# Performance work log

Hardware: AMD Instinct MI355X
Metric: run time of the kernel (lower is better)

Reference implementation:

```python
import jax, jax.numpy as jnp
import numpy as np

LEVELS = (4, 3, 2, 1)
EMBED = 4096


def _spp(x):
    # adaptive max pool to n x n per level (H,W divisible by every level), concat
    N, C, H, W = x.shape
    feats = []
    for n in LEVELS:
        p = x.reshape(N, C, n, H // n, n, W // n).max(axis=(3, 5))
        feats.append(p.reshape(N, C * n * n))
    return jnp.concatenate(feats, axis=1)  # (N, 90)


def _lstm_cell(x, h, c, wih, whh, bih, bhh):
    # torch gate order: i, f, g, o
    g = x @ wih.T + bih + h @ whh.T + bhh
    i, f, gg, o = jnp.split(g, 4, axis=-1)
    c2 = jax.nn.sigmoid(f) * c + jax.nn.sigmoid(i) * jnp.tanh(gg)
    h2 = jax.nn.sigmoid(o) * jnp.tanh(c2)
    return h2, c2


def _lin_init(key, out_d, in_d):
    k = 1.0 / np.sqrt(in_d)
    kw, kb = jax.random.split(key)
    w = jax.random.uniform(kw, (out_d, in_d), jnp.float32, -k, k)
    b = jax.random.uniform(kb, (out_d,), jnp.float32, -k, k)
    return w, b


def setup_inputs() -> dict:
    key = jax.random.key(0)
    ks = jax.random.split(key, 9)
    frames = jax.random.normal(ks[0], (8, 256, 3, 96, 96), jnp.float32)
    spp_fc_w, spp_fc_b = _lin_init(ks[1], EMBED, 90)
    fc7_w, fc7_b = _lin_init(ks[2], 64, EMBED)
    forecast_w, forecast_b = _lin_init(ks[3], 90, 32)
    fc8_w, fc8_b = _lin_init(ks[4], 1, 32)
    lstm1_wih, lstm1_bih = _lin_init(ks[5], 256, 64)
    lstm1_whh, lstm1_bhh = _lin_init(ks[6], 256, 64)
    lstm2_wih, lstm2_bih = _lin_init(ks[7], 128, 64)
    lstm2_whh, lstm2_bhh = _lin_init(ks[8], 128, 32)
    return dict(frames=frames, spp_fc_w=spp_fc_w, spp_fc_b=spp_fc_b,
                fc7_w=fc7_w, fc7_b=fc7_b,
                lstm1_wih=lstm1_wih, lstm1_whh=lstm1_whh, lstm1_bih=lstm1_bih, lstm1_bhh=lstm1_bhh,
                lstm2_wih=lstm2_wih, lstm2_whh=lstm2_whh, lstm2_bih=lstm2_bih, lstm2_bhh=lstm2_bhh,
                forecast_w=forecast_w, forecast_b=forecast_b, fc8_w=fc8_w, fc8_b=fc8_b)


def reference(frames, spp_fc_w, spp_fc_b, fc7_w, fc7_b,
              lstm1_wih, lstm1_whh, lstm1_bih, lstm1_bhh,
              lstm2_wih, lstm2_whh, lstm2_bih, lstm2_bhh,
              forecast_w, forecast_b, fc8_w, fc8_b):
    B, S, C, H, W = frames.shape
    pooled = _spp(frames.reshape(B * S, C, H, W))               # (B*S, 90)
    emb = jax.nn.relu(pooled @ spp_fc_w.T + spp_fc_b)           # (B*S, 4096)
    emb = jax.nn.relu(emb @ fc7_w.T + fc7_b).reshape(B, S, -1)  # (B, S, 64)

    def step(carry, e):
        h1, c1, h2, c2 = carry
        h1n, c1n = _lstm_cell(e, h1, c1, lstm1_wih, lstm1_whh, lstm1_bih, lstm1_bhh)
        h2n, c2n = _lstm_cell(h1n, h2, c2, lstm2_wih, lstm2_whh, lstm2_bih, lstm2_bhh)
        fpool = h2n @ forecast_w.T + forecast_b                  # (B, 90)
        fe = jax.nn.relu(fpool @ spp_fc_w.T + spp_fc_b)
        fe = jax.nn.relu(fe @ fc7_w.T + fc7_b)
        fh1, _ = _lstm_cell(fe, h1n, c1n, lstm1_wih, lstm1_whh, lstm1_bih, lstm1_bhh)
        fh2, _ = _lstm_cell(fh1, h2n, c2n, lstm2_wih, lstm2_whh, lstm2_bih, lstm2_bhh)
        return (h1n, c1n, h2n, c2n), (h2n, fh2, fpool)

    z = lambda d: jnp.zeros((B, d), frames.dtype)
    init = (z(64), z(64), z(32), z(32))
    _, (prog, fprog, fpooled) = jax.lax.scan(step, init, jnp.swapaxes(emb, 0, 1))
    prog = jnp.swapaxes(prog, 0, 1)        # (B, S, 32)
    fprog = jnp.swapaxes(fprog, 0, 1)      # (B, S, 32)
    fpooled = jnp.swapaxes(fpooled, 0, 1)  # (B, S, 90)
    progress = jax.nn.sigmoid(prog @ fc8_w.T + fc8_b)[..., 0]    # (B, S)
    fprogress = jax.nn.sigmoid(fprog @ fc8_w.T + fc8_b)[..., 0]  # (B, S)
    return (progress, fprogress, pooled.reshape(B, S, -1), fpooled)
```

## Files before the change

kernel.cpp:

```cpp
#include <hip/hip_runtime.h>
#include <math.h>

static const size_t OFF_POOLED = 0;
static const size_t OFF_EMB1   = 184320;
static const size_t OFF_ACC1   = OFF_EMB1 + 8388608;
static const size_t OFF_ACC2   = OFF_ACC1 + 131072;
static const size_t OFF_X1     = OFF_ACC2 + 131072;
static const size_t OFF_FPOOL  = OFF_X1 + 524288;
static const size_t OFF_H1     = OFF_FPOOL + 184320;
static const size_t OFF_C1     = OFF_H1 + 131072;
static const size_t OFF_H2     = OFF_C1 + 131072;
static const size_t OFF_C2     = OFF_H2 + 65536;

typedef _Float16 h2f_t __attribute__((ext_vector_type(2)));

__device__ __forceinline__ float fsig(float x) {
    return __builtin_amdgcn_rcpf(1.0f + __expf(-x));
}
__device__ __forceinline__ float ftanh(float x) {
    return 1.0f - 2.0f * __builtin_amdgcn_rcpf(__expf(2.0f * x) + 1.0f);
}

__device__ __forceinline__ float fdot2(h2f_t a, h2f_t b, float c) {
#if __has_builtin(__builtin_amdgcn_fdot2)
    return __builtin_amdgcn_fdot2(a, b, c, false);
#else
    return c + (float)a.x * (float)b.x + (float)a.y * (float)b.y;
#endif
}
__device__ __forceinline__ h2f_t h2pack(float x, float y) {
    h2f_t r; r.x = (_Float16)x; r.y = (_Float16)y; return r;
}
__device__ __forceinline__ h2f_t h2bits(int v) {
    return __builtin_bit_cast(h2f_t, v);
}
__device__ __forceinline__ void lds_fence() {
    asm volatile("s_waitcnt lgkmcnt(0)" ::: "memory");
}

__global__ __launch_bounds__(256) void spp_kernel(const float* __restrict__ frames,
                                                  float* __restrict__ out_pooled,
                                                  float* __restrict__ ws_pooled) {
    __shared__ __align__(16) float img[9216];
    __shared__ float p4[16], p3[9];
    int blk = blockIdx.x;
    int n = blk / 3, c = blk % 3;
    const float* src = frames + (size_t)blk * 9216;
    int tid = threadIdx.x;
    const float4* s4 = (const float4*)src;
    float4* i4 = (float4*)img;
#pragma unroll
    for (int j = 0; j < 9; ++j) i4[tid + 256 * j] = s4[tid + 256 * j];
    __syncthreads();
    {
        int r = tid >> 4, i = tid & 15;
        int ri = r >> 2, rj = r & 3;
        const float* base = &img[(24 * ri) * 96 + 24 * rj];
        float m = -3.402823466e38f;
#pragma unroll 6
        for (int k = 0; k < 36; ++k) {
            int e = i + 16 * k;
            int row = e / 24;
            int col = e - row * 24;
            m = fmaxf(m, base[row * 96 + col]);
        }
#pragma unroll
        for (int sh = 8; sh >= 1; sh >>= 1) m = fmaxf(m, __shfl_xor(m, sh));
        if (i == 0) p4[r] = m;
    }
    if (tid < 144) {
        int r = tid >> 4, i = tid & 15;
        int ri = r / 3, rj = r % 3;
        const float* base = &img[(32 * ri) * 96 + 32 * rj];
        float m = -3.402823466e38f;
#pragma unroll 8
        for (int k = 0; k < 64; ++k) {
            int e = i + 16 * k;
            int row = e >> 5, col = e & 31;
            m = fmaxf(m, base[row * 96 + col]);
        }
#pragma unroll
        for (int sh = 8; sh >= 1; sh >>= 1) m = fmaxf(m, __shfl_xor(m, sh));
        if (i == 0) p3[r] = m;
    }
    __syncthreads();
    if (tid < 30) {
        float v; int off;
        if (tid < 16) { v = p4[tid]; off = c * 16 + tid; }
        else if (tid < 25) { int q = tid - 16; v = p3[q]; off = 48 + c * 9 + q; }
        else if (tid < 29) {
            int q = tid - 25; int i2 = q >> 1, j2 = q & 1;
            v = fmaxf(fmaxf(p4[(2 * i2) * 4 + 2 * j2], p4[(2 * i2) * 4 + 2 * j2 + 1]),
                      fmaxf(p4[(2 * i2 + 1) * 4 + 2 * j2], p4[(2 * i2 + 1) * 4 + 2 * j2 + 1]));
            off = 75 + c * 4 + q;
        } else {
            float m = p4[0];
#pragma unroll
            for (int q = 1; q < 16; ++q) m = fmaxf(m, p4[q]);
            v = m; off = 87 + c;
        }
        out_pooled[(size_t)n * 90 + off] = v;
        ws_pooled[(size_t)n * 90 + off] = v;
    }
}

__global__ __launch_bounds__(256) void gemm90_kernel(const float* __restrict__ X,
                                                     const float* __restrict__ W,
                                                     const float* __restrict__ bias,
                                                     float* __restrict__ Y) {
    __shared__ __align__(16) float Xs[32][132];
    __shared__ __align__(16) float Ws[32][132];
    int tid = threadIdx.x;
    int R0 = blockIdx.x * 128, C0 = blockIdx.y * 128;
    int r0t = (tid >> 4) * 8, c0t = (tid & 15) * 8;
    float acc[8][8];
#pragma unroll
    for (int i = 0; i < 8; ++i)
#pragma unroll
        for (int j = 0; j < 8; ++j) acc[i][j] = 0.f;

    for (int k0 = 0; k0 < 96; k0 += 32) {
#pragma unroll
        for (int j = 0; j < 4; ++j) {
            int idx = tid + 256 * j;
            int row = idx & 127, q = idx >> 7;
            int kg = k0 + 4 * q;
            const float2* p = (const float2*)&X[(size_t)(R0 + row) * 90 + kg];
            float2 a = p[0], b = p[1];
            Xs[4 * q + 0][row] = a.x; Xs[4 * q + 1][row] = a.y;
            Xs[4 * q + 2][row] = b.x; Xs[4 * q + 3][row] = b.y;
        }
#pragma unroll
        for (int j = 0; j < 4; ++j) {
            int idx = tid + 256 * j;
            int col = idx & 127, q = idx >> 7;
            int kg = k0 + 4 * q;
            float v0, v1, v2, v3;
            if (kg + 3 < 90) {
                const float2* p = (const float2*)&W[(size_t)(C0 + col) * 90 + kg];
                float2 a = p[0], b = p[1];
                v0 = a.x; v1 = a.y; v2 = b.x; v3 = b.y;
            } else {
                const float* p = &W[(size_t)(C0 + col) * 90];
                v0 = (kg + 0 < 90) ? p[kg + 0] : 0.f;
                v1 = (kg + 1 < 90) ? p[kg + 1] : 0.f;
                v2 = (kg + 2 < 90) ? p[kg + 2] : 0.f;
                v3 = (kg + 3 < 90) ? p[kg + 3] : 0.f;
            }
            Ws[4 * q + 0][col] = v0; Ws[4 * q + 1][col] = v1;
            Ws[4 * q + 2][col] = v2; Ws[4 * q + 3][col] = v3;
        }
        __syncthreads();
#pragma unroll 8
        for (int kk = 0; kk < 32; ++kk) {
            float4 xa = *(const float4*)&Xs[kk][r0t];
            float4 xb = *(const float4*)&Xs[kk][r0t + 4];
            float4 wa = *(const float4*)&Ws[kk][c0t];
            float4 wb = *(const float4*)&Ws[kk][c0t + 4];
            float xr[8] = {xa.x, xa.y, xa.z, xa.w, xb.x, xb.y, xb.z, xb.w};
            float wc[8] = {wa.x, wa.y, wa.z, wa.w, wb.x, wb.y, wb.z, wb.w};
#pragma unroll
            for (int i = 0; i < 8; ++i)
#pragma unroll
                for (int j = 0; j < 8; ++j) acc[i][j] += xr[i] * wc[j];
        }
        __syncthreads();
    }
    float4 ba = *(const float4*)&bias[C0 + c0t];
    float4 bb = *(const float4*)&bias[C0 + c0t + 4];
    float bs[8] = {ba.x, ba.y, ba.z, ba.w, bb.x, bb.y, bb.z, bb.w};
#pragma unroll
    for (int i = 0; i < 8; ++i) {
        float4 o0, o1;
        o0.x = fmaxf(acc[i][0] + bs[0], 0.f); o0.y = fmaxf(acc[i][1] + bs[1], 0.f);
        o0.z = fmaxf(acc[i][2] + bs[2], 0.f); o0.w = fmaxf(acc[i][3] + bs[3], 0.f);
        o1.x = fmaxf(acc[i][4] + bs[4], 0.f); o1.y = fmaxf(acc[i][5] + bs[5], 0.f);
        o1.z = fmaxf(acc[i][6] + bs[6], 0.f); o1.w = fmaxf(acc[i][7] + bs[7], 0.f);
        *(float4*)&Y[(size_t)(R0 + r0t + i) * 4096 + C0 + c0t] = o0;
        *(float4*)&Y[(size_t)(R0 + r0t + i) * 4096 + C0 + c0t + 4] = o1;
    }
}

__global__ __launch_bounds__(256) void gemmk_kernel(const float* __restrict__ X,
                                                    const float* __restrict__ W,
                                                    float* __restrict__ acc_out) {
    __shared__ __align__(16) float Xs[32][132];
    __shared__ __align__(16) float Ws[32][68];
    int tid = threadIdx.x;
    int R0 = blockIdx.x * 128;
    int K0 = blockIdx.y * 256;
    int r0t = (tid >> 4) * 8, c0t = (tid & 15) * 4;
    float acc[8][4];
#pragma unroll
    for (int i = 0; i < 8; ++i)
#pragma unroll
        for (int j = 0; j < 4; ++j) acc[i][j] = 0.f;

    for (int k0 = K0; k0 < K0 + 256; k0 += 32) {
#pragma unroll
        for (int j = 0; j < 4; ++j) {
            int idx = tid + 256 * j;
            int row = idx & 127, q = idx >> 7;
            float4 a = *(const float4*)&X[(size_t)(R0 + row) * 4096 + k0 + 4 * q];
            Xs[4 * q + 0][row] = a.x; Xs[4 * q + 1][row] = a.y;
            Xs[4 * q + 2][row] = a.z; Xs[4 * q + 3][row] = a.w;
        }
#pragma unroll
        for (int j = 0; j < 2; ++j) {
            int idx = tid + 256 * j;
            int col = idx & 63, q = idx >> 6;
            float4 a = *(const float4*)&W[(size_t)col * 4096 + k0 + 4 * q];
            Ws[4 * q + 0][col] = a.x; Ws[4 * q + 1][col] = a.y;
            Ws[4 * q + 2][col] = a.z; Ws[4 * q + 3][col] = a.w;
        }
        __syncthreads();
#pragma unroll 8
        for (int kk = 0; kk < 32; ++kk) {
            float4 xa = *(const float4*)&Xs[kk][r0t];
            float4 xb = *(const float4*)&Xs[kk][r0t + 4];
            float4 wa = *(const float4*)&Ws[kk][c0t];
            float xr[8] = {xa.x, xa.y, xa.z, xa.w, xb.x, xb.y, xb.z, xb.w};
            float wc[4] = {wa.x, wa.y, wa.z, wa.w};
#pragma unroll
            for (int i = 0; i < 8; ++i)
#pragma unroll
                for (int j = 0; j < 4; ++j) acc[i][j] += xr[i] * wc[j];
        }
        __syncthreads();
    }
#pragma unroll
    for (int i = 0; i < 8; ++i)
#pragma unroll
        for (int j = 0; j < 4; ++j)
            atomicAdd(&acc_out[(size_t)(R0 + r0t + i) * 64 + c0t + j], acc[i][j]);
}

__global__ __launch_bounds__(256) void x1_kernel(const float* __restrict__ acc1,
                                                 const float* __restrict__ fc7_b,
                                                 const float* __restrict__ wih1,
                                                 const float* __restrict__ bih1,
                                                 const float* __restrict__ bhh1,
                                                 float* __restrict__ X1) {
    __shared__ __align__(16) float xr[8][64];
    int tid = threadIdx.x;
    int R0 = blockIdx.x * 8;
#pragma unroll
    for (int j = 0; j < 2; ++j) {
        int idx = tid + 256 * j;
        int r = idx >> 6, k = idx & 63;
        xr[r][k] = fmaxf(acc1[(size_t)(R0 + r) * 64 + k] + fc7_b[k], 0.f);
    }
    __syncthreads();
    int u = tid;
    float w[64];
#pragma unroll
    for (int q = 0; q < 16; ++q) {
        float4 a = *(const float4*)&wih1[(size_t)u * 64 + 4 * q];
        w[4 * q] = a.x; w[4 * q + 1] = a.y; w[4 * q + 2] = a.z; w[4 * q + 3] = a.w;
    }
    float bias = bih1[u] + bhh1[u];
    for (int r = 0; r < 8; ++r) {
        float g = bias;
#pragma unroll
        for (int k = 0; k < 64; ++k) g += w[k] * xr[r][k];
        X1[(size_t)(R0 + r) * 256 + u] = g;
    }
}

__global__ __launch_bounds__(64, 1) void seq_kernel(const float* __restrict__ X1,
                                                    const float* __restrict__ whh1,
                                                    const float* __restrict__ wih2,
                                                    const float* __restrict__ whh2,
                                                    const float* __restrict__ bih2,
                                                    const float* __restrict__ bhh2,
                                                    float* __restrict__ h1_all, float* __restrict__ c1_all,
                                                    float* __restrict__ h2_all, float* __restrict__ c2_all) {
    __shared__ __align__(16) _Float16 h1h[64];
    __shared__ __align__(16) _Float16 h2h[32];
    const int l = threadIdx.x;
    const size_t n0 = (size_t)blockIdx.x * 256;

    h2f_t w1[4][32];
#pragma unroll
    for (int g = 0; g < 4; ++g) {
        const float* wr = whh1 + (size_t)(g * 64 + l) * 64;
#pragma unroll
        for (int q = 0; q < 32; ++q) w1[g][q] = h2pack(wr[2 * q], wr[2 * q + 1]);
    }
    h2f_t w2a[2][32], w2b[2][16];
#pragma unroll
    for (int g = 0; g < 2; ++g) {
        const float* wa = wih2 + (size_t)(g * 64 + l) * 64;
#pragma unroll
        for (int q = 0; q < 32; ++q) w2a[g][q] = h2pack(wa[2 * q], wa[2 * q + 1]);
        const float* wb = whh2 + (size_t)(g * 64 + l) * 32;
#pragma unroll
        for (int q = 0; q < 16; ++q) w2b[g][q] = h2pack(wb[2 * q], wb[2 * q + 1]);
    }
    const float b2a = bih2[l] + bhh2[l];
    const float b2b = bih2[64 + l] + bhh2[64 + l];

    const float* xp = X1 + n0 * 256;
    float c1, c2 = 0.f, pa, pb;
    {
        float a0 = xp[l], a1 = xp[64 + l], a2 = xp[128 + l], a3 = xp[192 + l];
        (void)a1;
        c1 = fsig(a0) * ftanh(a2);
        float h1n = fsig(a3) * ftanh(c1);
        h1h[l] = (_Float16)h1n;
        h1_all[n0 * 64 + l] = h1n;
        c1_all[n0 * 64 + l] = c1;
        pa = b2a; pb = b2b;
    }
    lds_fence();
    float xb0[4], xb1[4];
    {
        const float* x1r = xp + 256;
        xb0[0] = x1r[l]; xb0[1] = x1r[64 + l]; xb0[2] = x1r[128 + l]; xb0[3] = x1r[192 + l];
        const float* x2r = xp + 512;
        xb1[0] = x2r[l]; xb1[1] = x2r[64 + l]; xb1[2] = x2r[128 + l]; xb1[3] = x2r[192 + l];
    }

#pragma unroll 2
    for (int t = 0; t < 256; ++t) {
        int4 hv[8];
        const int4* h1v = (const int4*)h1h;
#pragma unroll
        for (int q = 0; q < 8; ++q) hv[q] = h1v[q];
        float* xc = (t & 1) ? xb1 : xb0;
        float a0 = xc[0], a1 = xc[1], a2 = xc[2], a3 = xc[3];
        {
            int tr = (t + 3 < 256) ? (t + 3) : 255;
            const float* xq = xp + (size_t)tr * 256;
            xc[0] = xq[l]; xc[1] = xq[64 + l]; xc[2] = xq[128 + l]; xc[3] = xq[192 + l];
        }
#pragma unroll
        for (int q = 0; q < 8; ++q) {
            int4 v = hv[q];
            h2f_t hh0 = h2bits(v.x), hh1 = h2bits(v.y), hh2 = h2bits(v.z), hh3 = h2bits(v.w);
            a0 = fdot2(w1[0][4 * q], hh0, a0); a1 = fdot2(w1[1][4 * q], hh0, a1);
            a2 = fdot2(w1[2][4 * q], hh0, a2); a3 = fdot2(w1[3][4 * q], hh0, a3);
            pa = fdot2(w2a[0][4 * q], hh0, pa); pb = fdot2(w2a[1][4 * q], hh0, pb);
            a0 = fdot2(w1[0][4 * q + 1], hh1, a0); a1 = fdot2(w1[1][4 * q + 1], hh1, a1);
            a2 = fdot2(w1[2][4 * q + 1], hh1, a2); a3 = fdot2(w1[3][4 * q + 1], hh1, a3);
            pa = fdot2(w2a[0][4 * q + 1], hh1, pa); pb = fdot2(w2a[1][4 * q + 1], hh1, pb);
            a0 = fdot2(w1[0][4 * q + 2], hh2, a0); a1 = fdot2(w1[1][4 * q + 2], hh2, a1);
            a2 = fdot2(w1[2][4 * q + 2], hh2, a2); a3 = fdot2(w1[3][4 * q + 2], hh2, a3);
            pa = fdot2(w2a[0][4 * q + 2], hh2, pa); pb = fdot2(w2a[1][4 * q + 2], hh2, pb);
            a0 = fdot2(w1[0][4 * q + 3], hh3, a0); a1 = fdot2(w1[1][4 * q + 3], hh3, a1);
            a2 = fdot2(w1[2][4 * q + 3], hh3, a2); a3 = fdot2(w1[3][4 * q + 3], hh3, a3);
            pa = fdot2(w2a[0][4 * q + 3], hh3, pa); pb = fdot2(w2a[1][4 * q + 3], hh3, pb);
        }
        float gf_ = __shfl(pa, (l & 31) + 32);
        float go_ = __shfl(pb, (l & 31) + 32);
        if (l < 32) {
            c2 = fsig(gf_) * c2 + fsig(pa) * ftanh(pb);
            float h2n = fsig(go_) * ftanh(c2);
            h2h[l] = (_Float16)h2n;
            h2_all[(n0 + t) * 32 + l] = h2n;
            c2_all[(n0 + t) * 32 + l] = c2;
        }
        lds_fence();
        c1 = fsig(a1) * c1 + fsig(a0) * ftanh(a2);
        float h1n = fsig(a3) * ftanh(c1);
        h1h[l] = (_Float16)h1n;
        if (t < 255) {
            h1_all[(n0 + t + 1) * 64 + l] = h1n;
            c1_all[(n0 + t + 1) * 64 + l] = c1;
        }
        pa = b2a; pb = b2b;
        const int4* h2v = (const int4*)h2h;
#pragma unroll
        for (int q = 0; q < 4; ++q) {
            int4 v = h2v[q];
            h2f_t hh0 = h2bits(v.x), hh1 = h2bits(v.y), hh2 = h2bits(v.z), hh3 = h2bits(v.w);
            pa = fdot2(w2b[0][4 * q], hh0, pa); pb = fdot2(w2b[1][4 * q], hh0, pb);
            pa = fdot2(w2b[0][4 * q + 1], hh1, pa); pb = fdot2(w2b[1][4 * q + 1], hh1, pb);
            pa = fdot2(w2b[0][4 * q + 2], hh2, pa); pb = fdot2(w2b[1][4 * q + 2], hh2, pb);
            pa = fdot2(w2b[0][4 * q + 3], hh3, pa); pb = fdot2(w2b[1][4 * q + 3], hh3, pb);
        }
        lds_fence();
    }
}

__global__ __launch_bounds__(256) void fpool_kernel(const float* __restrict__ h2_all,
                                                    const float* __restrict__ fw,
                                                    const float* __restrict__ fb,
                                                    const float* __restrict__ fc8_w,
                                                    const float* __restrict__ fc8_b,
                                                    float* __restrict__ fpool_ws,
                                                    float* __restrict__ out_fpooled,
                                                    float* __restrict__ out_progress) {
    __shared__ __align__(16) float h2t[16][32];
    __shared__ float fwl[2880];
    int tid = threadIdx.x;
    int R0 = blockIdx.x * 16;
#pragma unroll
    for (int j = 0; j < 2; ++j) {
        int idx = tid + 256 * j;
        int r = idx >> 5, k = idx & 31;
        h2t[r][k] = h2_all[(size_t)(R0 + r) * 32 + k];
    }
    for (int idx = tid; idx < 2880; idx += 256) fwl[idx] = fw[idx];
    __syncthreads();
    for (int j = 0; j < 6; ++j) {
        int idx = tid + 256 * j;
        if (idx < 1440) {
            int r = idx / 90, cc = idx % 90;
            float g = fb[cc];
#pragma unroll
            for (int k = 0; k < 32; ++k) g += h2t[r][k] * fwl[cc * 32 + k];
            fpool_ws[(size_t)(R0 + r) * 90 + cc] = g;
            out_fpooled[(size_t)(R0 + r) * 90 + cc] = g;
        }
    }
    if (tid < 16) {
        float g = fc8_b[0];
#pragma unroll
        for (int k = 0; k < 32; ++k) g += h2t[tid][k] * fc8_w[k];
        out_progress[R0 + tid] = fsig(g);
    }
}

__global__ __launch_bounds__(256) void fh_kernel(const float* __restrict__ acc2,
                                                 const float* __restrict__ fc7_b,
                                                 const float* __restrict__ h1_all,
                                                 const float* __restrict__ c1_all,
                                                 const float* __restrict__ h2_all,
                                                 const float* __restrict__ c2_all,
                                                 const float* __restrict__ wih1,
                                                 const float* __restrict__ whh1,
                                                 const float* __restrict__ bih1,
                                                 const float* __restrict__ bhh1,
                                                 const float* __restrict__ wih2,
                                                 const float* __restrict__ whh2,
                                                 const float* __restrict__ bih2,
                                                 const float* __restrict__ bhh2,
                                                 const float* __restrict__ fc8_w,
                                                 const float* __restrict__ fc8_b,
                                                 float* __restrict__ out_fprog) {
    __shared__ __align__(16) float xcat[8][128];
    __shared__ float g1f[8][256];
    __shared__ __align__(16) float x2c[8][96];
    __shared__ float g2f[8][128];
    __shared__ __align__(16) float fh2s[8][32];
    int tid = threadIdx.x;
    int R0 = blockIdx.x * 8;
#pragma unroll
    for (int j = 0; j < 4; ++j) {
        int idx = tid + 256 * j;
        int r = idx >> 7, k = idx & 127;
        float v;
        if (k < 64) v = fmaxf(acc2[(size_t)(R0 + r) * 64 + k] + fc7_b[k], 0.f);
        else v = h1_all[(size_t)(R0 + r) * 64 + (k - 64)];
        xcat[r][k] = v;
    }
    {
        int r = tid >> 5, k = tid & 31;
        x2c[r][64 + k] = h2_all[(size_t)(R0 + r) * 32 + k];
    }
    __syncthreads();
    {
        int u = tid;
        float wa[64], wb[64];
#pragma unroll
        for (int q = 0; q < 16; ++q) {
            float4 a = *(const float4*)&wih1[(size_t)u * 64 + 4 * q];
            wa[4 * q] = a.x; wa[4 * q + 1] = a.y; wa[4 * q + 2] = a.z; wa[4 * q + 3] = a.w;
            float4 b = *(const float4*)&whh1[(size_t)u * 64 + 4 * q];
            wb[4 * q] = b.x; wb[4 * q + 1] = b.y; wb[4 * q + 2] = b.z; wb[4 * q + 3] = b.w;
        }
        float bias = bih1[u] + bhh1[u];
        for (int r = 0; r < 8; ++r) {
            float g = bias;
#pragma unroll
            for (int k = 0; k < 64; ++k) g += wa[k] * xcat[r][k];
#pragma unroll
            for (int k = 0; k < 64; ++k) g += wb[k] * xcat[r][64 + k];
            g1f[r][u] = g;
        }
    }
    __syncthreads();
#pragma unroll
    for (int j = 0; j < 2; ++j) {
        int idx = tid + 256 * j;
        int r = idx >> 6, h = idx & 63;
        float gi = g1f[r][h], gf = g1f[r][64 + h], gg = g1f[r][128 + h], go = g1f[r][192 + h];
        float c1v = c1_all[(size_t)(R0 + r) * 64 + h];
        float c = fsig(gf) * c1v + fsig(gi) * ftanh(gg);
        x2c[r][h] = fsig(go) * ftanh(c);
    }
    __syncthreads();
    {
        int u = tid & 127;
        int rb = (tid >> 7) * 4;
        float wa[64], wb2[32];
#pragma unroll
        for (int q = 0; q < 16; ++q) {
            float4 a = *(const float4*)&wih2[(size_t)u * 64 + 4 * q];
            wa[4 * q] = a.x; wa[4 * q + 1] = a.y; wa[4 * q + 2] = a.z; wa[4 * q + 3] = a.w;
        }
#pragma unroll
        for (int q = 0; q < 8; ++q) {
            float4 b = *(const float4*)&whh2[(size_t)u * 32 + 4 * q];
            wb2[4 * q] = b.x; wb2[4 * q + 1] = b.y; wb2[4 * q + 2] = b.z; wb2[4 * q + 3] = b.w;
        }
        float bias = bih2[u] + bhh2[u];
        for (int r = rb; r < rb + 4; ++r) {
            float g = bias;
#pragma unroll
            for (int k = 0; k < 64; ++k) g += wa[k] * x2c[r][k];
#pragma unroll
            for (int k = 0; k < 32; ++k) g += wb2[k] * x2c[r][64 + k];
            g2f[r][u] = g;
        }
    }
    __syncthreads();
    {
        int r = tid >> 5, v = tid & 31;
        float gi = g2f[r][v], gf = g2f[r][32 + v], gg = g2f[r][64 + v], go = g2f[r][96 + v];
        float c2v = c2_all[(size_t)(R0 + r) * 32 + v];
        float c = fsig(gf) * c2v + fsig(gi) * ftanh(gg);
        fh2s[r][v] = fsig(go) * ftanh(c);
    }
    __syncthreads();
    if (tid < 8) {
        float g = fc8_b[0];
#pragma unroll
        for (int k = 0; k < 32; ++k) g += fh2s[tid][k] * fc8_w[k];
        out_fprog[R0 + tid] = fsig(g);
    }
}

extern "C" void kernel_launch(void* const* d_in, const int* in_sizes, int n_in,
                              void* d_out, int out_size, void* d_ws, size_t ws_size,
                              hipStream_t stream) {
    (void)in_sizes; (void)n_in; (void)out_size; (void)ws_size;
    const float* frames   = (const float*)d_in[0];
    const float* spp_fc_w = (const float*)d_in[1];
    const float* spp_fc_b = (const float*)d_in[2];
    const float* fc7_w    = (const float*)d_in[3];
    const float* fc7_b    = (const float*)d_in[4];
    const float* l1_wih   = (const float*)d_in[5];
    const float* l1_whh   = (const float*)d_in[6];
    const float* l1_bih   = (const float*)d_in[7];
    const float* l1_bhh   = (const float*)d_in[8];
    const float* l2_wih   = (const float*)d_in[9];
    const float* l2_whh   = (const float*)d_in[10];
    const float* l2_bih   = (const float*)d_in[11];
    const float* l2_bhh   = (const float*)d_in[12];
    const float* fo_w     = (const float*)d_in[13];
    const float* fo_b     = (const float*)d_in[14];
    const float* fc8_w    = (const float*)d_in[15];
    const float* fc8_b    = (const float*)d_in[16];
    float* out = (float*)d_out;
    float* ws  = (float*)d_ws;

    float* pooled = ws + OFF_POOLED;
    float* emb1   = ws + OFF_EMB1;
    float* acc1   = ws + OFF_ACC1;
    float* acc2   = ws + OFF_ACC2;
    float* X1     = ws + OFF_X1;
    float* fpool  = ws + OFF_FPOOL;
    float* h1a    = ws + OFF_H1;
    float* c1a    = ws + OFF_C1;
    float* h2a    = ws + OFF_H2;
    float* c2a    = ws + OFF_C2;

    float* out_prog    = out;
    float* out_fprog   = out + 2048;
    float* out_pooled  = out + 4096;
    float* out_fpooled = out + 188416;

    hipMemsetAsync(acc1, 0, (size_t)262144 * sizeof(float), stream);
    spp_kernel<<<6144, 256, 0, stream>>>(frames, out_pooled, pooled);
    gemm90_kernel<<<dim3(16, 32), 256, 0, stream>>>(pooled, spp_fc_w, spp_fc_b, emb1);
    gemmk_kernel<<<dim3(16, 16), 256, 0, stream>>>(emb1, fc7_w, acc1);
    x1_kernel<<<256, 256, 0, stream>>>(acc1, fc7_b, l1_wih, l1_bih, l1_bhh, X1);
    seq_kernel<<<8, 64, 0, stream>>>(X1, l1_whh, l2_wih, l2_whh, l2_bih, l2_bhh, h1a, c1a, h2a, c2a);
    fpool_kernel<<<128, 256, 0, stream>>>(h2a, fo_w, fo_b, fc8_w, fc8_b, fpool, out_fpooled, out_prog);
    gemm90_kernel<<<dim3(16, 32), 256, 0, stream>>>(fpool, spp_fc_w, spp_fc_b, emb1);
    gemmk_kernel<<<dim3(16, 16), 256, 0, stream>>>(emb1, fc7_w, acc2);
    fh_kernel<<<256, 256, 0, stream>>>(acc2, fc7_b, h1a, c1a, h2a, c2a,
                                       l1_wih, l1_whh, l1_bih, l1_bhh,
                                       l2_wih, l2_whh, l2_bih, l2_bhh,
                                       fc8_w, fc8_b, out_fprog);
}
```

Baseline: 769.1 us.

## Split sequential LSTM kernel into two wavefronts pipelining layer 1 and layer 2

The sequential LSTM kernel now launches 128 threads. One wavefront runs the layer-1 recurrence and writes h1 into a double-buffered LDS slot. The second wavefront computes layer 2 for the previous step, and the two hand off through per-step barriers. Dot products are split across several independent accumulators to shorten dependency chains, and v_permlane32_swap replaces the shuffles used to gather gates. This takes layer-2 work off the layer-1 critical path, at the cost of a workgroup barrier every timestep and reliance on the correctness of the partial lgkmcnt wait.

```diff
diff --git a/kernel.cpp b/kernel.cpp
--- a/kernel.cpp
+++ b/kernel.cpp
@@ -36,6 +36,9 @@
 }
 __device__ __forceinline__ void lds_fence() {
     asm volatile("s_waitcnt lgkmcnt(0)" ::: "memory");
+}
+__device__ __forceinline__ void permswap(float& x, float& y) {
+    asm volatile("v_permlane32_swap_b32 %0, %1" : "+v"(x), "+v"(y));
 }
 
 __global__ __launch_bounds__(256) void spp_kernel(const float* __restrict__ frames,
@@ -267,119 +270,171 @@
     }
 }
 
-__global__ __launch_bounds__(64, 1) void seq_kernel(const float* __restrict__ X1,
-                                                    const float* __restrict__ whh1,
-                                                    const float* __restrict__ wih2,
-                                                    const float* __restrict__ whh2,
-                                                    const float* __restrict__ bih2,
-                                                    const float* __restrict__ bhh2,
-                                                    float* __restrict__ h1_all, float* __restrict__ c1_all,
-                                                    float* __restrict__ h2_all, float* __restrict__ c2_all) {
-    __shared__ __align__(16) _Float16 h1h[64];
+__global__ __launch_bounds__(128, 1) void seq_kernel(const float* __restrict__ X1,
+                                                     const float* __restrict__ whh1,
+                                                     const float* __restrict__ wih2,
+                                                     const float* __restrict__ whh2,
+                                                     const float* __restrict__ bih2,
+                                                     const float* __restrict__ bhh2,
+                                                     float* __restrict__ h1_all, float* __restrict__ c1_all,
+                                                     float* __restrict__ h2_all, float* __restrict__ c2_all) {
+    __shared__ __align__(16) _Float16 h1h[2][64];
     __shared__ __align__(16) _Float16 h2h[32];
-    const int l = threadIdx.x;
+    const int tid = threadIdx.x;
+    const int l = tid & 63;
     const size_t n0 = (size_t)blockIdx.x * 256;
-
-    h2f_t w1[4][32];
-#pragma unroll
-    for (int g = 0; g < 4; ++g) {
-        const float* wr = whh1 + (size_t)(g * 64 + l) * 64;
-#pragma unroll
-        for (int q = 0; q < 32; ++q) w1[g][q] = h2pack(wr[2 * q], wr[2 * q + 1]);
-    }
-    h2f_t w2a[2][32], w2b[2][16];
-#pragma unroll
-    for (int g = 0; g < 2; ++g) {
-        const float* wa = wih2 + (size_t)(g * 64 + l) * 64;
-#pragma unroll
-        for (int q = 0; q < 32; ++q) w2a[g][q] = h2pack(wa[2 * q], wa[2 * q + 1]);
-        const float* wb = whh2 + (size_t)(g * 64 + l) * 32;
-#pragma unroll
-        for (int q = 0; q < 16; ++q) w2b[g][q] = h2pack(wb[2 * q], wb[2 * q + 1]);
-    }
-    const float b2a = bih2[l] + bhh2[l];
-    const float b2b = bih2[64 + l] + bhh2[64 + l];
-
     const float* xp = X1 + n0 * 256;
-    float c1, c2 = 0.f, pa, pb;
-    {
-        float a0 = xp[l], a1 = xp[64 + l], a2 = xp[128 + l], a3 = xp[192 + l];
-        (void)a1;
-        c1 = fsig(a0) * ftanh(a2);
-        float h1n = fsig(a3) * ftanh(c1);
-        h1h[l] = (_Float16)h1n;
-        h1_all[n0 * 64 + l] = h1n;
-        c1_all[n0 * 64 + l] = c1;
-        pa = b2a; pb = b2b;
-    }
-    lds_fence();
-    float xb0[4], xb1[4];
-    {
-        const float* x1r = xp + 256;
-        xb0[0] = x1r[l]; xb0[1] = x1r[64 + l]; xb0[2] = x1r[128 + l]; xb0[3] = x1r[192 + l];
-        const float* x2r = xp + 512;
-        xb1[0] = x2r[l]; xb1[1] = x2r[64 + l]; xb1[2] = x2r[128 + l]; xb1[3] = x2r[192 + l];
-    }
+
+    if (tid < 64) {
+        h2f_t w1[4][32];
+#pragma unroll
+        for (int g = 0; g < 4; ++g) {
+            const float* wr = whh1 + (size_t)(g * 64 + l) * 64;
+#pragma unroll
+            for (int q = 0; q < 32; ++q) w1[g][q] = h2pack(wr[2 * q], wr[2 * q + 1]);
+        }
+        float c1;
+        {
+            float a0 = xp[l], a1 = xp[64 + l], a2 = xp[128 + l], a3 = xp[192 + l];
+            (void)a1;
+            c1 = fsig(a0) * ftanh(a2);
+            float h1n = fsig(a3) * ftanh(c1);
+            h1h[0][l] = (_Float16)h1n;
+            h1_all[n0 * 64 + l] = h1n;
+            c1_all[n0 * 64 + l] = c1;
+        }
+        float xb0[4], xb1[4];
+        {
+            const float* x1r = xp + 256;
+            xb0[0] = x1r[l]; xb0[1] = x1r[64 + l]; xb0[2] = x1r[128 + l]; xb0[3] = x1r[192 + l];
+            const float* x2r = xp + 512;
+            xb1[0] = x2r[l]; xb1[1] = x2r[64 + l]; xb1[2] = x2r[128 + l]; xb1[3] = x2r[192 + l];
+        }
+        lds_fence();
+        int4 hv[8];
+        {
+            const int4* hb = (const int4*)&h1h[0][0];
+#pragma unroll
+            for (int q = 0; q < 8; ++q) hv[q] = hb[q];
+        }
+        __builtin_amdgcn_s_barrier();
 
 #pragma unroll 2
-    for (int t = 0; t < 256; ++t) {
-        int4 hv[8];
-        const int4* h1v = (const int4*)h1h;
-#pragma unroll
-        for (int q = 0; q < 8; ++q) hv[q] = h1v[q];
-        float* xc = (t & 1) ? xb1 : xb0;
-        float a0 = xc[0], a1 = xc[1], a2 = xc[2], a3 = xc[3];
+        for (int t = 0; t < 256; ++t) {
+            float* xc = (t & 1) ? xb1 : xb0;
+            float a0 = xc[0], a1 = xc[1], a2 = xc[2], a3 = xc[3];
+            {
+                int tr = (t + 3 < 256) ? (t + 3) : 255;
+                const float* xq = xp + (size_t)tr * 256;
+                xc[0] = xq[l]; xc[1] = xq[64 + l]; xc[2] = xq[128 + l]; xc[3] = xq[192 + l];
+            }
+            float b0 = 0.f, b1 = 0.f, b2 = 0.f, b3 = 0.f;
+#pragma unroll
+            for (int q = 0; q < 8; ++q) {
+                int4 v = hv[q];
+                h2f_t hh0 = h2bits(v.x), hh1 = h2bits(v.y), hh2 = h2bits(v.z), hh3 = h2bits(v.w);
+                a0 = fdot2(w1[0][4 * q], hh0, a0);     a1 = fdot2(w1[1][4 * q], hh0, a1);
+                a2 = fdot2(w1[2][4 * q], hh0, a2);     a3 = fdot2(w1[3][4 * q], hh0, a3);
+                b0 = fdot2(w1[0][4 * q + 1], hh1, b0); b1 = fdot2(w1[1][4 * q + 1], hh1, b1);
+                b2 = fdot2(w1[2][4 * q + 1], hh1, b2); b3 = fdot2(w1[3][4 * q + 1], hh1, b3);
+                a0 = fdot2(w1[0][4 * q + 2], hh2, a0); a1 = fdot2(w1[1][4 * q + 2], hh2, a1);
+                a2 = fdot2(w1[2][4 * q + 2], hh2, a2); a3 = fdot2(w1[3][4 * q + 2], hh2, a3);
+                b0 = fdot2(w1[0][4 * q + 3], hh3, b0); b1 = fdot2(w1[1][4 * q + 3], hh3, b1);
+                b2 = fdot2(w1[2][4 * q + 3], hh3, b2); b3 = fdot2(w1[3][4 * q + 3], hh3, b3);
+            }
+            a0 += b0; a1 += b1; a2 += b2; a3 += b3;
+            c1 = fsig(a1) * c1 + fsig(a0) * ftanh(a2);
+            float h1n = fsig(a3) * ftanh(c1);
+            h1h[(t + 1) & 1][l] = (_Float16)h1n;
+            if (t < 255) {
+                h1_all[(n0 + t + 1) * 64 + l] = h1n;
+                c1_all[(n0 + t + 1) * 64 + l] = c1;
+            }
+            {
+                const int4* hb = (const int4*)&h1h[(t + 1) & 1][0];
+#pragma unroll
+                for (int q = 0; q < 8; ++q) hv[q] = hb[q];
+            }
+            asm volatile("s_waitcnt lgkmcnt(8)" ::: "memory");
+            __builtin_amdgcn_s_barrier();
+        }
+    } else {
+        h2f_t w2a[2][32], w2b[2][16];
+#pragma unroll
+        for (int g = 0; g < 2; ++g) {
+            const float* wa = wih2 + (size_t)(g * 64 + l) * 64;
+#pragma unroll
+            for (int q = 0; q < 32; ++q) w2a[g][q] = h2pack(wa[2 * q], wa[2 * q + 1]);
+            const float* wb = whh2 + (size_t)(g * 64 + l) * 32;
+#pragma unroll
+            for (int q = 0; q < 16; ++q) w2b[g][q] = h2pack(wb[2 * q], wb[2 * q + 1]);
+        }
+        const float b2a = bih2[l] + bhh2[l];
+        const float b2b = bih2[64 + l] + bhh2[64 + l];
+        const bool hi = (l >= 32);
+        if (l < 32) h2h[l] = (_Float16)0.f;
+        lds_fence();
+        int4 gv[4];
         {
-            int tr = (t + 3 < 256) ? (t + 3) : 255;
-            const float* xq = xp + (size_t)tr * 256;
-            xc[0] = xq[l]; xc[1] = xq[64 + l]; xc[2] = xq[128 + l]; xc[3] = xq[192 + l];
-        }
-#pragma unroll
-        for (int q = 0; q < 8; ++q) {
-            int4 v = hv[q];
-            h2f_t hh0 = h2bits(v.x), hh1 = h2bits(v.y), hh2 = h2bits(v.z), hh3 = h2bits(v.w);
-            a0 = fdot2(w1[0][4 * q], hh0, a0); a1 = fdot2(w1[1][4 * q], hh0, a1);
-            a2 = fdot2(w1[2][4 * q], hh0, a2); a3 = fdot2(w1[3][4 * q], hh0, a3);
-            pa = fdot2(w2a[0][4 * q], hh0, pa); pb = fdot2(w2a[1][4 * q], hh0, pb);
-            a0 = fdot2(w1[0][4 * q + 1], hh1, a0); a1 = fdot2(w1[1][4 * q + 1], hh1, a1);
-            a2 = fdot2(w1[2][4 * q + 1], hh1, a2); a3 = fdot2(w1[3][4 * q + 1], hh1, a3);
-            pa = fdot2(w2a[0][4 * q + 1], hh1, pa); pb = fdot2(w2a[1][4 * q + 1], hh1, pb);
-            a0 = fdot2(w1[0][4 * q + 2], hh2, a0); a1 = fdot2(w1[1][4 * q + 2], hh2, a1);
-            a2 = fdot2(w1[2][4 * q + 2], hh2, a2); a3 = fdot2(w1[3][4 * q + 2], hh2, a3);
-            pa = fdot2(w2a[0][4 * q + 2], hh2, pa); pb = fdot2(w2a[1][4 * q + 2], hh2, pb);
-            a0 = fdot2(w1[0][4 * q + 3], hh3, a0); a1 = fdot2(w1[1][4 * q + 3], hh3, a1);
-            a2 = fdot2(w1[2][4 * q + 3], hh3, a2); a3 = fdot2(w1[3][4 * q + 3], hh3, a3);
-            pa = fdot2(w2a[0][4 * q + 3], hh3, pa); pb = fdot2(w2a[1][4 * q + 3], hh3, pb);
-        }
-        float gf_ = __shfl(pa, (l & 31) + 32);
-        float go_ = __shfl(pb, (l & 31) + 32);
-        if (l < 32) {
-            c2 = fsig(gf_) * c2 + fsig(pa) * ftanh(pb);
-            float h2n = fsig(go_) * ftanh(c2);
-            h2h[l] = (_Float16)h2n;
-            h2_all[(n0 + t) * 32 + l] = h2n;
-            c2_all[(n0 + t) * 32 + l] = c2;
-        }
-        lds_fence();
-        c1 = fsig(a1) * c1 + fsig(a0) * ftanh(a2);
-        float h1n = fsig(a3) * ftanh(c1);
-        h1h[l] = (_Float16)h1n;
-        if (t < 255) {
-            h1_all[(n0 + t + 1) * 64 + l] = h1n;
-            c1_all[(n0 + t + 1) * 64 + l] = c1;
-        }
-        pa = b2a; pb = b2b;
-        const int4* h2v = (const int4*)h2h;
-#pragma unroll
-        for (int q = 0; q < 4; ++q) {
-            int4 v = h2v[q];
-            h2f_t hh0 = h2bits(v.x), hh1 = h2bits(v.y), hh2 = h2bits(v.z), hh3 = h2bits(v.w);
-            pa = fdot2(w2b[0][4 * q], hh0, pa); pb = fdot2(w2b[1][4 * q], hh0, pb);
-            pa = fdot2(w2b[0][4 * q + 1], hh1, pa); pb = fdot2(w2b[1][4 * q + 1], hh1, pb);
-            pa = fdot2(w2b[0][4 * q + 2], hh2, pa); pb = fdot2(w2b[1][4 * q + 2], hh2, pb);
-            pa = fdot2(w2b[0][4 * q + 3], hh3, pa); pb = fdot2(w2b[1][4 * q + 3], hh3, pb);
-        }
-        lds_fence();
+            const int4* gb = (const int4*)&h2h[0];
+#pragma unroll
+            for (int q = 0; q < 4; ++q) gv[q] = gb[q];
+        }
+        float c2 = 0.f;
+        __builtin_amdgcn_s_barrier();
+
+        for (int t = 0; t < 256; ++t) {
+            int4 hv[8];
+            {
+                const int4* hb = (const int4*)&h1h[t & 1][0];
+#pragma unroll
+                for (int q = 0; q < 8; ++q) hv[q] = hb[q];
+            }
+            float pa = b2a, pb = b2b, pc = 0.f, pd = 0.f;
+            float pe = 0.f, pf = 0.f, pg = 0.f, ph = 0.f;
+#pragma unroll
+            for (int q = 0; q < 4; ++q) {
+                int4 u = gv[q];
+                h2f_t gg0 = h2bits(u.x), gg1 = h2bits(u.y), gg2 = h2bits(u.z), gg3 = h2bits(u.w);
+                pe = fdot2(w2b[0][4 * q], gg0, pe);     pf = fdot2(w2b[1][4 * q], gg0, pf);
+                pg = fdot2(w2b[0][4 * q + 1], gg1, pg); ph = fdot2(w2b[1][4 * q + 1], gg1, ph);
+                pe = fdot2(w2b[0][4 * q + 2], gg2, pe); pf = fdot2(w2b[1][4 * q + 2], gg2, pf);
+                pg = fdot2(w2b[0][4 * q + 3], gg3, pg); ph = fdot2(w2b[1][4 * q + 3], gg3, ph);
+            }
+#pragma unroll
+            for (int q = 0; q < 8; ++q) {
+                int4 v = hv[q];
+                h2f_t hh0 = h2bits(v.x), hh1 = h2bits(v.y), hh2 = h2bits(v.z), hh3 = h2bits(v.w);
+                pa = fdot2(w2a[0][4 * q], hh0, pa);     pb = fdot2(w2a[1][4 * q], hh0, pb);
+                pa = fdot2(w2a[0][4 * q + 1], hh1, pa); pb = fdot2(w2a[1][4 * q + 1], hh1, pb);
+                pc = fdot2(w2a[0][4 * q + 2], hh2, pc); pd = fdot2(w2a[1][4 * q + 2], hh2, pd);
+                pc = fdot2(w2a[0][4 * q + 3], hh3, pc); pd = fdot2(w2a[1][4 * q + 3], hh3, pd);
+            }
+            pa = (pa + pc) + (pe + pg);
+            pb = (pb + pd) + (pf + ph);
+            float s1a = pa, s1b = pb;
+            permswap(s1a, s1b);
+            float s2a = pb, s2b = pa;
+            permswap(s2a, s2b);
+            float gi = hi ? s2a : s1a;
+            float gf = hi ? s2b : s1b;
+            float gg = hi ? s1a : s2a;
+            float go = hi ? s1b : s2b;
+            c2 = fsig(gf) * c2 + fsig(gi) * ftanh(gg);
+            float h2n = fsig(go) * ftanh(c2);
+            if (l < 32) {
+                h2h[l] = (_Float16)h2n;
+                h2_all[(n0 + t) * 32 + l] = h2n;
+                c2_all[(n0 + t) * 32 + l] = c2;
+            }
+            lds_fence();
+            {
+                const int4* gb = (const int4*)&h2h[0];
+#pragma unroll
+                for (int q = 0; q < 4; ++q) gv[q] = gb[q];
+            }
+            __builtin_amdgcn_s_barrier();
+        }
     }
 }
 
@@ -577,7 +632,7 @@
     gemm90_kernel<<<dim3(16, 32), 256, 0, stream>>>(pooled, spp_fc_w, spp_fc_b, emb1);
     gemmk_kernel<<<dim3(16, 16), 256, 0, stream>>>(emb1, fc7_w, acc1);
     x1_kernel<<<256, 256, 0, stream>>>(acc1, fc7_b, l1_wih, l1_bih, l1_bhh, X1);
-    seq_kernel<<<8, 64, 0, stream>>>(X1, l1_whh, l2_wih, l2_whh, l2_bih, l2_bhh, h1a, c1a, h2a, c2a);
+    seq_kernel<<<8, 128, 0, stream>>>(X1, l1_whh, l2_wih, l2_whh, l2_bih, l2_bhh, h1a, c1a, h2a, c2a);
     fpool_kernel<<<128, 256, 0, stream>>>(h2a, fo_w, fo_b, fc8_w, fc8_b, fpool, out_fpooled, out_prog);
     gemm90_kernel<<<dim3(16, 32), 256, 0, stream>>>(fpool, spp_fc_w, spp_fc_b, emb1);
     gemmk_kernel<<<dim3(16, 16), 256, 0, stream>>>(emb1, fc7_w, acc2);
```

Result: faster. 669.5 us (-12.9%).
